# Kernel tuning notes

Measured on AMD Instinct MI355X. Metric: run time of the kernel, lower is better.

## Reference

```python
import jax, jax.numpy as jnp
import numpy as np

B, S, F = 128, 256, 40
H, D, NH, L, FF = 64, 128, 4, 2, 2048
REG, BIN, NW = 8, 1, 3
NEG = -1e9


def _ln(x, s, b, eps=1e-5):
    m = x.mean(-1, keepdims=True)
    v = ((x - m) ** 2).mean(-1, keepdims=True)
    return (x - m) / jnp.sqrt(v + eps) * s + b


def setup_inputs() -> dict:
    key = jax.random.key(0)
    ks = list(jax.random.split(key, 40))
    k = iter(ks)
    def rn(shape, s=0.05):
        return jax.random.normal(next(k), shape, jnp.float32) * s
    inp = {}
    inp['x'] = jax.random.normal(next(k), (B, S, F), jnp.float32)
    inp['mask'] = jnp.ones((B, S, F), jnp.float32)
    inp['delta'] = jax.random.uniform(next(k), (B, S, F), jnp.float32)
    # GRU params (torch layout: [3H, in], gates order r,z,n)
    inp['gru_w_ih'] = rn((3 * H, 3 * F))
    inp['gru_w_hh'] = rn((3 * H, H))
    inp['gru_b_ih'] = rn((3 * H,))
    inp['gru_b_hh'] = rn((3 * H,))
    inp['dm_w'] = rn((D, H)); inp['dm_b'] = rn((D,))
    # transformer layers stacked on leading dim L
    inp['in_proj_w'] = rn((L, 3 * D, D)); inp['in_proj_b'] = rn((L, 3 * D))
    inp['out_proj_w'] = rn((L, D, D)); inp['out_proj_b'] = rn((L, D))
    inp['lin1_w'] = rn((L, FF, D)); inp['lin1_b'] = rn((L, FF))
    inp['lin2_w'] = rn((L, D, FF)); inp['lin2_b'] = rn((L, D))
    inp['ln1_s'] = jnp.ones((L, D), jnp.float32); inp['ln1_b'] = jnp.zeros((L, D), jnp.float32)
    inp['ln2_s'] = jnp.ones((L, D), jnp.float32); inp['ln2_b'] = jnp.zeros((L, D), jnp.float32)
    inp['score_w'] = rn((1, D)); inp['score_b'] = rn((1,))
    inp['reg_w'] = rn((NW, REG, D)); inp['reg_b'] = rn((NW, REG))
    inp['bin_w'] = rn((NW, BIN, D)); inp['bin_b'] = rn((NW, BIN))
    inp['window_id'] = jax.random.randint(next(k), (B,), 0, NW, jnp.int32)
    return inp


def reference(x, mask, delta, gru_w_ih, gru_w_hh, gru_b_ih, gru_b_hh, dm_w, dm_b,
              in_proj_w, in_proj_b, out_proj_w, out_proj_b, lin1_w, lin1_b,
              lin2_w, lin2_b, ln1_s, ln1_b, ln2_s, ln2_b, score_w, score_b,
              reg_w, reg_b, bin_w, bin_b, window_id):
    inp = jnp.concatenate([x, mask, delta], -1)          # [B,S,3F]
    xw = inp @ gru_w_ih.T + gru_b_ih                      # [B,S,3H] precomputed input gates

    def step(h, xw_t):
        gh = h @ gru_w_hh.T + gru_b_hh
        xr, xz, xn = jnp.split(xw_t, 3, -1)
        hr, hz, hn = jnp.split(gh, 3, -1)
        r = jax.nn.sigmoid(xr + hr)
        zg = jax.nn.sigmoid(xz + hz)
        n = jnp.tanh(xn + r * hn)
        h_new = (1.0 - zg) * n + zg * h
        return h_new, h_new

    h0 = jnp.zeros((x.shape[0], H), x.dtype)
    _, hs = jax.lax.scan(step, h0, jnp.swapaxes(xw, 0, 1))  # [S,B,H]
    z = jnp.swapaxes(hs, 0, 1) @ dm_w.T + dm_b              # [B,S,D]

    time_mask = mask.sum(-1) > 0                            # [B,S] bool
    bias = jnp.where(time_mask[:, None, None, :], 0.0, NEG).astype(z.dtype)
    dh = D // NH
    scale = 1.0 / np.sqrt(dh)

    for l in range(L):  # post-LN torch TransformerEncoderLayer
        qkv = z @ in_proj_w[l].T + in_proj_b[l]
        q, k, v = jnp.split(qkv, 3, -1)
        q = q.reshape(B, S, NH, dh).transpose(0, 2, 1, 3)
        k = k.reshape(B, S, NH, dh).transpose(0, 2, 1, 3)
        v = v.reshape(B, S, NH, dh).transpose(0, 2, 1, 3)
        attn = jax.nn.softmax(jnp.einsum('bhqd,bhkd->bhqk', q, k) * scale + bias, -1)
        o = jnp.einsum('bhqk,bhkd->bhqd', attn, v).transpose(0, 2, 1, 3).reshape(B, S, D)
        z = _ln(z + (o @ out_proj_w[l].T + out_proj_b[l]), ln1_s[l], ln1_b[l])
        ff = jax.nn.relu(z @ lin1_w[l].T + lin1_b[l]) @ lin2_w[l].T + lin2_b[l]
        z = _ln(z + ff, ln2_s[l], ln2_b[l])

    scores = (z @ score_w.T + score_b)[..., 0]              # [B,S]
    scores = jnp.where(time_mask, scores, NEG)
    alpha = jax.nn.softmax(scores, 1)
    pooled = jnp.einsum('bsd,bs->bd', z, alpha)             # [B,D]

    # routed heads: gather 1-of-3 head weights per sample, batched matvec
    y_reg = jnp.einsum('bod,bd->bo', reg_w[window_id], pooled) + reg_b[window_id]
    y_bin = jnp.einsum('bod,bd->bo', bin_w[window_id], pooled) + bin_b[window_id]
    return (y_reg, y_bin)
```

## Files before the change

### kernel.cpp

```cpp
#include <hip/hip_runtime.h>

typedef __attribute__((ext_vector_type(8))) short short8;
typedef __attribute__((ext_vector_type(4))) float f32x4;
typedef unsigned short u16;

#define BB   128
#define SS   256
#define FIN  40
#define HH   64
#define DD   128
#define NHH  4
#define LL   2
#define NEGV (-1e9f)

__device__ __forceinline__ u16 f2b(float f) {
    unsigned u = __float_as_uint(f);
    return (u16)((u + 0x7FFFu + ((u >> 16) & 1u)) >> 16);
}
__device__ __forceinline__ float b2f(u16 u) {
    return __uint_as_float(((unsigned)u) << 16);
}

__device__ __forceinline__ void gl_lds16(const void* g, void* s) {
    __builtin_amdgcn_global_load_lds(
        (const __attribute__((address_space(1))) void*)g,
        (__attribute__((address_space(3))) void*)s, 16, 0, 0);
}

__global__ __launch_bounds__(192) void xw_kernel(const float* __restrict__ x,
                                                 const float* __restrict__ mask,
                                                 const float* __restrict__ delta,
                                                 const float* __restrict__ w_ih,
                                                 const float* __restrict__ b_ih,
                                                 float* __restrict__ xwt) {
    __shared__ float inp[16][120];
    __shared__ float wl[192][21];
    int group = blockIdx.x >> 8;
    int t = blockIdx.x & 255;
    int tid = threadIdx.x;

    for (int idx = tid; idx < 16 * 120; idx += 192) {
        int r = idx / 120, k = idx % 120;
        size_t g = (size_t)(group * 16 + r) * 256 + t;
        float v;
        if (k < 40)      v = x[g * FIN + k];
        else if (k < 80) v = mask[g * FIN + (k - 40)];
        else             v = delta[g * FIN + (k - 80)];
        inp[r][k] = v;
    }

    float acc[16];
#pragma unroll
    for (int r = 0; r < 16; ++r) acc[r] = 0.f;

    for (int kt = 0; kt < 6; ++kt) {
        __syncthreads();
        for (int idx = tid; idx < 192 * 20; idx += 192) {
            int r = idx / 20, k = idx % 20;
            wl[r][k] = w_ih[(size_t)r * 120 + kt * 20 + k];
        }
        __syncthreads();
#pragma unroll
        for (int kk = 0; kk < 20; ++kk) {
            float w = wl[tid][kk];
            int kg = kt * 20 + kk;
#pragma unroll
            for (int r = 0; r < 16; ++r) acc[r] += w * inp[r][kg];
        }
    }
    float bias = b_ih[tid];
    float* o = xwt + ((size_t)(group * 256 + t) * 192 + tid) * 16;
#pragma unroll
    for (int r = 0; r < 16; r += 4) {
        float4 v = {acc[r] + bias, acc[r + 1] + bias, acc[r + 2] + bias, acc[r + 3] + bias};
        *(float4*)&o[r] = v;
    }
}

__device__ __forceinline__ float gru_gate(float xr, float xz, float xn,
                                          float ar, float az, float an, float hold) {
    float r  = 1.f / (1.f + __expf(-(xr + ar)));
    float zg = 1.f / (1.f + __expf(-(xz + az)));
    float nx = xn + r * an;
    float n  = 2.f / (1.f + __expf(-2.f * nx)) - 1.f;
    return (1.f - zg) * n + zg * hold;
}

__global__ __launch_bounds__(512, 1) void pre_kernel(const float* __restrict__ w_hh,
                                                     const float* __restrict__ b_hh,
                                                     const float* __restrict__ xwt,
                                                     u16* __restrict__ hsb,
                                                     const float* __restrict__ dm_w,
                                                     const float* __restrict__ ip_w,
                                                     const float* __restrict__ op_w,
                                                     const float* __restrict__ l1_w,
                                                     const float* __restrict__ l2_w,
                                                     u16* __restrict__ o_dm, u16* __restrict__ o_ip,
                                                     u16* __restrict__ o_op, u16* __restrict__ o_l1,
                                                     u16* __restrict__ o_l2,
                                                     const float* __restrict__ mask,
                                                     float* __restrict__ tm) {
    __shared__ __align__(16) u16 hb[2][16 * 64];
    __shared__ __align__(16) u16 hstage[8][16 * 64];
    int blk = blockIdx.x;
    int tid = threadIdx.x;

    if (blk >= 8) {
        if (blk < 298) {
            int cb = blk - 8;
            const float* s; u16* d; int off;
            if      (cb < 2)   { s = dm_w; d = o_dm; off = cb; }
            else if (cb < 26)  { s = ip_w; d = o_ip; off = cb - 2; }
            else if (cb < 34)  { s = op_w; d = o_op; off = cb - 26; }
            else if (cb < 162) { s = l1_w; d = o_l1; off = cb - 34; }
            else               { s = l2_w; d = o_l2; off = cb - 162; }
            int i = (off * 512 + tid) * 8;
            float4 a = *(const float4*)&s[i];
            float4 b = *(const float4*)&s[i + 4];
            short8 o;
            o[0] = (short)f2b(a.x); o[1] = (short)f2b(a.y); o[2] = (short)f2b(a.z); o[3] = (short)f2b(a.w);
            o[4] = (short)f2b(b.x); o[5] = (short)f2b(b.y); o[6] = (short)f2b(b.z); o[7] = (short)f2b(b.w);
            *(short8*)&d[i] = o;
        } else {
            int row = (blk - 298) * 512 + tid;
            if (row < BB * SS) {
                const float* m = mask + (size_t)row * FIN;
                float s = 0.f;
                for (int f = 0; f < FIN; ++f) s += m[f];
                tm[row] = (s > 0.f) ? 1.f : 0.f;
            }
        }
        return;
    }

    int b0 = blk * 16;
    int w = tid >> 6, lane = tid & 63;
    int fr = lane & 15, hi = lane >> 4;
    int cw = w & 3;
    int jg = w >> 2;

    for (int idx = tid; idx < 1024; idx += 512) hb[0][idx] = 0;

    int c = cw * 16 + fr;
    float br_ = b_hh[c], bz_ = b_hh[64 + c], bn_ = b_hh[128 + c];

    short8 wfr[2], wfz[2], wfn[2];
#pragma unroll
    for (int ks = 0; ks < 2; ++ks) {
        int slot = ks * 4 + hi;
        const float* p0 = w_hh + (size_t)c * 64 + slot * 8;
        const float* p1 = w_hh + (size_t)(64 + c) * 64 + slot * 8;
        const float* p2 = w_hh + (size_t)(128 + c) * 64 + slot * 8;
#pragma unroll
        for (int q = 0; q < 8; ++q) {
            wfr[ks][q] = (short)f2b(p0[q]);
            wfz[ks][q] = (short)f2b(p1[q]);
            wfn[ks][q] = (short)f2b(p2[q]);
        }
    }

    const float* xg = xwt + (size_t)blk * (256 * 192 * 16);
    int lo = hi * 4 + jg * 2;

    float hrA = 0.f, hrB = 0.f;

    int woA = (lo + 0) * 64 + ((((c >> 3) ^ ((lo + 0) & 7))) << 3) + (c & 7);
    int woB = (lo + 1) * 64 + ((((c >> 3) ^ ((lo + 1) & 7))) << 3) + (c & 7);
    int soA = (lo + 0) * 64 + c;
    int soB = (lo + 1) * 64 + c;

    float2 pxr[4], pxz[4], pxn[4];
#pragma unroll
    for (int u = 0; u < 4; ++u) {
        pxr[u] = *(const float2*)&xg[((size_t)u * 192 + c) * 16 + lo];
        pxz[u] = *(const float2*)&xg[((size_t)u * 192 + 64 + c) * 16 + lo];
        pxn[u] = *(const float2*)&xg[((size_t)u * 192 + 128 + c) * 16 + lo];
    }
    __syncthreads();

    int cur = 0;
    auto step = [&](float2 xr2, float2 xz2, float2 xn2, int ts) {
        f32x4 ar = {br_, br_, br_, br_};
        f32x4 az = {bz_, bz_, bz_, bz_};
        f32x4 an = {bn_, bn_, bn_, bn_};
#pragma unroll
        for (int ks = 0; ks < 2; ++ks) {
            int soff = (((ks << 2) + hi) ^ (fr & 7)) << 3;
            short8 af = *(const short8*)&hb[cur][fr * 64 + soff];
            ar = __builtin_amdgcn_mfma_f32_16x16x32_bf16(af, wfr[ks], ar, 0, 0, 0);
            az = __builtin_amdgcn_mfma_f32_16x16x32_bf16(af, wfz[ks], az, 0, 0, 0);
            an = __builtin_amdgcn_mfma_f32_16x16x32_bf16(af, wfn[ks], an, 0, 0, 0);
        }
        float aR0, aR1, aZ0, aZ1, aN0, aN1;
        if (jg == 0) { aR0 = ar[0]; aR1 = ar[1]; aZ0 = az[0]; aZ1 = az[1]; aN0 = an[0]; aN1 = an[1]; }
        else         { aR0 = ar[2]; aR1 = ar[3]; aZ0 = az[2]; aZ1 = az[3]; aN0 = an[2]; aN1 = an[3]; }
        hrA = gru_gate(xr2.x, xz2.x, xn2.x, aR0, aZ0, aN0, hrA);
        hrB = gru_gate(xr2.y, xz2.y, xn2.y, aR1, aZ1, aN1, hrB);
        u16 v0 = f2b(hrA), v1 = f2b(hrB);
        int nxt = cur ^ 1;
        hb[nxt][woA] = v0; hb[nxt][woB] = v1;
        hstage[ts][soA] = v0; hstage[ts][soB] = v1;
        asm volatile("s_waitcnt lgkmcnt(0)\n\ts_barrier" ::: "memory");
        cur = nxt;
    };

    for (int t = 0; t < SS; t += 8) {
#pragma unroll
        for (int u = 0; u < 8; ++u) {
            int tp = t + u + 4; tp = (tp < SS) ? tp : (SS - 1);
            float2 nr = *(const float2*)&xg[((size_t)tp * 192 + c) * 16 + lo];
            float2 nz = *(const float2*)&xg[((size_t)tp * 192 + 64 + c) * 16 + lo];
            float2 nn = *(const float2*)&xg[((size_t)tp * 192 + 128 + c) * 16 + lo];
            step(pxr[u & 3], pxz[u & 3], pxn[u & 3], u);
            pxr[u & 3] = nr; pxz[u & 3] = nz; pxn[u & 3] = nn;
        }
#pragma unroll
        for (int f = 0; f < 2; ++f) {
            int idx = tid + f * 512;
            int c8 = idx & 7, pair = idx >> 3;
            int ts = pair >> 4, row = pair & 15;
            short8 v = *(const short8*)&hstage[ts][row * 64 + c8 * 8];
            *(short8*)&hsb[((size_t)(b0 + row) * SS + t + ts) * 64 + c8 * 8] = v;
        }
        asm volatile("s_waitcnt lgkmcnt(0)\n\ts_barrier" ::: "memory");
    }
}

__global__ __launch_bounds__(256, 1) void dmqkv_kernel(const u16* __restrict__ hsb,
                                                       const u16* __restrict__ dmw,
                                                       const float* __restrict__ dmb,
                                                       const u16* __restrict__ ipw,
                                                       const float* __restrict__ ipb,
                                                       float* __restrict__ z,
                                                       u16* __restrict__ qkvb) {
    __shared__ __align__(16) u16 ZB[2][128 * 64];
    __shared__ __align__(16) u16 W1C[2][128 * 64];
    int bm = blockIdx.x;
    int tid = threadIdx.x;
    int w = tid >> 6, lane = tid & 63;
    int wrow = (w >> 1) * 64, wcol = (w & 1) * 64;
    int fr = lane & 15, hi = lane >> 4;
    int rl = lane >> 3, ssl = (lane & 7) ^ rl;
    int swz = fr & 7;

#pragma unroll
    for (int i = 0; i < 4; ++i) {
        int ch = w * 4 + i, row = ch * 8 + rl;
        gl_lds16(hsb + ((size_t)(bm * 128 + row)) * 64 + ssl * 8, &ZB[0][ch * 512]);
        gl_lds16(dmw + ((size_t)row) * 64 + ssl * 8, &W1C[0][ch * 512]);
    }
    __syncthreads();

    f32x4 acc[4][4];
#pragma unroll
    for (int m = 0; m < 4; ++m)
#pragma unroll
        for (int n = 0; n < 4; ++n) acc[m][n] = (f32x4){0.f, 0.f, 0.f, 0.f};
#pragma unroll
    for (int kk = 0; kk < 2; ++kk) {
        int soff = (((kk << 2) + hi) ^ swz) << 3;
        short8 a[4], b[4];
#pragma unroll
        for (int m = 0; m < 4; ++m)
            a[m] = *(const short8*)&ZB[0][(wrow + m * 16 + fr) * 64 + soff];
#pragma unroll
        for (int n = 0; n < 4; ++n)
            b[n] = *(const short8*)&W1C[0][(wcol + n * 16 + fr) * 64 + soff];
#pragma unroll
        for (int m = 0; m < 4; ++m)
#pragma unroll
            for (int n = 0; n < 4; ++n)
                acc[m][n] = __builtin_amdgcn_mfma_f32_16x16x32_bf16(a[m], b[n], acc[m][n], 0, 0, 0);
    }
    __syncthreads();

    float bv[4];
#pragma unroll
    for (int n = 0; n < 4; ++n) bv[n] = dmb[wcol + n * 16 + fr];
#pragma unroll
    for (int m = 0; m < 4; ++m)
#pragma unroll
        for (int j = 0; j < 4; ++j) {
            int lrow = wrow + m * 16 + hi * 4 + j;
            int row = bm * 128 + lrow;
#pragma unroll
            for (int n = 0; n < 4; ++n) {
                int col = wcol + n * 16 + fr;
                float o = acc[m][n][j] + bv[n];
                z[(size_t)row * 128 + col] = o;
                int e = col & 63;
                ZB[col >> 6][lrow * 64 + ((((e >> 3) ^ (lrow & 7))) << 3) + (e & 7)] = f2b(o);
            }
        }
    __syncthreads();

    for (int bn = 0; bn < 3; ++bn) {
#pragma unroll
        for (int hk = 0; hk < 2; ++hk)
#pragma unroll
            for (int i = 0; i < 4; ++i) {
                int ch = w * 4 + i, row = ch * 8 + rl;
                gl_lds16(ipw + ((size_t)(bn * 128 + row)) * 128 + hk * 64 + ssl * 8, &W1C[hk][ch * 512]);
            }
        __syncthreads();

        f32x4 aq[4][4];
#pragma unroll
        for (int m = 0; m < 4; ++m)
#pragma unroll
            for (int n = 0; n < 4; ++n) aq[m][n] = (f32x4){0.f, 0.f, 0.f, 0.f};
#pragma unroll
        for (int ks = 0; ks < 4; ++ks) {
            int hk = ks >> 1;
            int soff = ((((ks & 1) << 2) + hi) ^ swz) << 3;
            short8 a[4], b[4];
#pragma unroll
            for (int m = 0; m < 4; ++m)
                a[m] = *(const short8*)&ZB[hk][(wrow + m * 16 + fr) * 64 + soff];
#pragma unroll
            for (int n = 0; n < 4; ++n)
                b[n] = *(const short8*)&W1C[hk][(wcol + n * 16 + fr) * 64 + soff];
#pragma unroll
            for (int m = 0; m < 4; ++m)
#pragma unroll
                for (int n = 0; n < 4; ++n)
                    aq[m][n] = __builtin_amdgcn_mfma_f32_16x16x32_bf16(a[m], b[n], aq[m][n], 0, 0, 0);
        }
        float qb[4];
#pragma unroll
        for (int n = 0; n < 4; ++n) qb[n] = ipb[bn * 128 + wcol + n * 16 + fr];
#pragma unroll
        for (int m = 0; m < 4; ++m)
#pragma unroll
            for (int j = 0; j < 4; ++j) {
                int row = bm * 128 + wrow + m * 16 + hi * 4 + j;
#pragma unroll
                for (int n = 0; n < 4; ++n)
                    qkvb[(size_t)row * 384 + bn * 128 + wcol + n * 16 + fr] = f2b(aq[m][n][j] + qb[n]);
            }
        __syncthreads();
    }
}

template <bool DO_QKV>
__global__ __launch_bounds__(256, 1) void tailqkv_kernel(const u16* __restrict__ attnob,
                                                         const u16* __restrict__ opw,
                                                         const float* __restrict__ opb,
                                                         const float* __restrict__ ln1s,
                                                         const float* __restrict__ ln1b,
                                                         const u16* __restrict__ w1,
                                                         const float* __restrict__ b1,
                                                         const u16* __restrict__ w2,
                                                         const float* __restrict__ b2,
                                                         const float* __restrict__ lns,
                                                         const float* __restrict__ lnb,
                                                         const u16* __restrict__ ipw,
                                                         const float* __restrict__ ipb,
                                                         float* __restrict__ z,
                                                         u16* __restrict__ qkvb) {
    __shared__ __align__(16) u16 ZB[2][128 * 64];
    __shared__ __align__(16) u16 W1C[2][128 * 64];
    __shared__ __align__(16) u16 W2C[2][128 * 64];
    __shared__ __align__(16) u16 A1[2][128 * 64];
    __shared__ float lred[2][2][128];
    int bm = blockIdx.x;
    int tid = threadIdx.x;
    int w = tid >> 6, lane = tid & 63;
    int wrow = (w >> 1) * 64, wcol = (w & 1) * 64;
    int fr = lane & 15, hi = lane >> 4;
    int rl = lane >> 3, ssl = (lane & 7) ^ rl;
    int swz = fr & 7;
    int xh = wrow >> 6;

#pragma unroll
    for (int hk = 0; hk < 2; ++hk)
#pragma unroll
        for (int i = 0; i < 4; ++i) {
            int ch = w * 4 + i, row = ch * 8 + rl;
            gl_lds16(attnob + ((size_t)(bm * 128 + row)) * 128 + hk * 64 + ssl * 8, &ZB[hk][ch * 512]);
            gl_lds16(opw + ((size_t)row) * 128 + hk * 64 + ssl * 8, &W1C[hk][ch * 512]);
        }
    __syncthreads();

    {
        f32x4 acc1[4][4];
#pragma unroll
        for (int m = 0; m < 4; ++m)
#pragma unroll
            for (int n = 0; n < 4; ++n) acc1[m][n] = (f32x4){0.f, 0.f, 0.f, 0.f};
#pragma unroll
        for (int ks = 0; ks < 4; ++ks) {
            int hk = ks >> 1;
            int soff = ((((ks & 1) << 2) + hi) ^ swz) << 3;
            short8 a[4], b[4];
#pragma unroll
            for (int m = 0; m < 4; ++m)
                a[m] = *(const short8*)&ZB[hk][(wrow + m * 16 + fr) * 64 + soff];
#pragma unroll
            for (int n = 0; n < 4; ++n)
                b[n] = *(const short8*)&W1C[hk][(wcol + n * 16 + fr) * 64 + soff];
#pragma unroll
            for (int m = 0; m < 4; ++m)
#pragma unroll
                for (int n = 0; n < 4; ++n)
                    acc1[m][n] = __builtin_amdgcn_mfma_f32_16x16x32_bf16(a[m], b[n], acc1[m][n], 0, 0, 0);
        }

        float bv[4];
#pragma unroll
        for (int n = 0; n < 4; ++n) bv[n] = opb[wcol + n * 16 + fr];
        float v[4][4][4];
#pragma unroll
        for (int m = 0; m < 4; ++m)
#pragma unroll
            for (int j = 0; j < 4; ++j) {
                int row = bm * 128 + wrow + m * 16 + hi * 4 + j;
#pragma unroll
                for (int n = 0; n < 4; ++n)
                    v[m][n][j] = acc1[m][n][j] + bv[n] + z[(size_t)row * 128 + wcol + n * 16 + fr];
            }
#pragma unroll
        for (int m = 0; m < 4; ++m)
#pragma unroll
            for (int j = 0; j < 4; ++j) {
                float s = v[m][0][j] + v[m][1][j] + v[m][2][j] + v[m][3][j];
                float q = v[m][0][j]*v[m][0][j] + v[m][1][j]*v[m][1][j]
                        + v[m][2][j]*v[m][2][j] + v[m][3][j]*v[m][3][j];
#pragma unroll
                for (int off = 1; off <= 8; off <<= 1) {
                    s += __shfl_xor(s, off);
                    q += __shfl_xor(q, off);
                }
                if (fr == 0) {
                    int lrow = wrow + m * 16 + hi * 4 + j;
                    lred[0][w & 1][lrow] = s;
                    lred[1][w & 1][lrow] = q;
                }
            }
        __syncthreads();
        float sv[4], bb[4];
#pragma unroll
        for (int n = 0; n < 4; ++n) {
            sv[n] = ln1s[wcol + n * 16 + fr];
            bb[n] = ln1b[wcol + n * 16 + fr];
        }
#pragma unroll
        for (int m = 0; m < 4; ++m)
#pragma unroll
            for (int j = 0; j < 4; ++j) {
                int lrow = wrow + m * 16 + hi * 4 + j;
                float mean = (lred[0][0][lrow] + lred[0][1][lrow]) * (1.f / 128.f);
                float msq  = (lred[1][0][lrow] + lred[1][1][lrow]) * (1.f / 128.f);
                float rstd = rsqrtf(msq - mean * mean + 1e-5f);
                int row = bm * 128 + lrow;
#pragma unroll
                for (int n = 0; n < 4; ++n) {
                    int col = wcol + n * 16 + fr;
                    float o = (v[m][n][j] - mean) * rstd * sv[n] + bb[n];
                    z[(size_t)row * 128 + col] = o;
                    int e = col & 63;
                    ZB[col >> 6][lrow * 64 + ((((e >> 3) ^ (lrow & 7))) << 3) + (e & 7)] = f2b(o);
                }
            }
    }
    __syncthreads();

    f32x4 acc2[4][4];
#pragma unroll
    for (int m = 0; m < 4; ++m)
#pragma unroll
        for (int n = 0; n < 4; ++n) acc2[m][n] = (f32x4){0.f, 0.f, 0.f, 0.f};

    for (int ci = 0; ci < 16; ++ci) {
#pragma unroll
        for (int hk = 0; hk < 2; ++hk)
#pragma unroll
            for (int i = 0; i < 4; ++i) {
                int ch = w * 4 + i, row = ch * 8 + rl;
                gl_lds16(w1 + ((size_t)(ci * 128 + row)) * 128 + hk * 64 + ssl * 8, &W1C[hk][ch * 512]);
                gl_lds16(w2 + ((size_t)row) * 2048 + ci * 128 + hk * 64 + ssl * 8, &W2C[hk][ch * 512]);
            }
        __syncthreads();

        f32x4 acc1[4][4];
#pragma unroll
        for (int m = 0; m < 4; ++m)
#pragma unroll
            for (int n = 0; n < 4; ++n) acc1[m][n] = (f32x4){0.f, 0.f, 0.f, 0.f};
#pragma unroll
        for (int ks = 0; ks < 4; ++ks) {
            int hk = ks >> 1;
            int soff = ((((ks & 1) << 2) + hi) ^ swz) << 3;
            short8 a[4], b[4];
#pragma unroll
            for (int m = 0; m < 4; ++m)
                a[m] = *(const short8*)&W1C[hk][(wrow + m * 16 + fr) * 64 + soff];
#pragma unroll
            for (int n = 0; n < 4; ++n)
                b[n] = *(const short8*)&ZB[hk][(wcol + n * 16 + fr) * 64 + soff];
#pragma unroll
            for (int m = 0; m < 4; ++m)
#pragma unroll
                for (int n = 0; n < 4; ++n)
                    acc1[m][n] = __builtin_amdgcn_mfma_f32_16x16x32_bf16(a[m], b[n], acc1[m][n], 0, 0, 0);
        }
#pragma unroll
        for (int m = 0; m < 4; ++m) {
            int x0 = wrow + m * 16 + hi * 4;
            float4 bb = *(const float4*)&b1[ci * 128 + x0];
            int slot = (x0 & 63) >> 3;
            int wadd = x0 & 7;
#pragma unroll
            for (int n = 0; n < 4; ++n) {
                int r = wcol + n * 16 + fr;
                float v0 = fmaxf(acc1[m][n][0] + bb.x, 0.f);
                float v1 = fmaxf(acc1[m][n][1] + bb.y, 0.f);
                float v2 = fmaxf(acc1[m][n][2] + bb.z, 0.f);
                float v3 = fmaxf(acc1[m][n][3] + bb.w, 0.f);
                uint2 pk;
                pk.x = (unsigned)f2b(v0) | ((unsigned)f2b(v1) << 16);
                pk.y = (unsigned)f2b(v2) | ((unsigned)f2b(v3) << 16);
                *(uint2*)&A1[xh][r * 64 + ((slot ^ (r & 7)) << 3) + wadd] = pk;
            }
        }
        __syncthreads();

#pragma unroll
        for (int ks = 0; ks < 4; ++ks) {
            int hk = ks >> 1;
            int soff = ((((ks & 1) << 2) + hi) ^ swz) << 3;
            short8 a[4], b[4];
#pragma unroll
            for (int m = 0; m < 4; ++m)
                a[m] = *(const short8*)&W2C[hk][(wrow + m * 16 + fr) * 64 + soff];
#pragma unroll
            for (int n = 0; n < 4; ++n)
                b[n] = *(const short8*)&A1[hk][(wcol + n * 16 + fr) * 64 + soff];
#pragma unroll
            for (int m = 0; m < 4; ++m)
#pragma unroll
                for (int n = 0; n < 4; ++n)
                    acc2[m][n] = __builtin_amdgcn_mfma_f32_16x16x32_bf16(a[m], b[n], acc2[m][n], 0, 0, 0);
        }
        __syncthreads();
    }

    float vv[4][4][4];
#pragma unroll
    for (int m = 0; m < 4; ++m) {
        int x0 = wrow + m * 16 + hi * 4;
        float4 bb = *(const float4*)&b2[x0];
#pragma unroll
        for (int n = 0; n < 4; ++n) {
            int y = wcol + n * 16 + fr;
            float4 zo = *(const float4*)&z[((size_t)(bm * 128 + y)) * 128 + x0];
            vv[m][n][0] = acc2[m][n][0] + bb.x + zo.x;
            vv[m][n][1] = acc2[m][n][1] + bb.y + zo.y;
            vv[m][n][2] = acc2[m][n][2] + bb.z + zo.z;
            vv[m][n][3] = acc2[m][n][3] + bb.w + zo.w;
        }
    }
#pragma unroll
    for (int n = 0; n < 4; ++n) {
        float s = 0.f, q = 0.f;
#pragma unroll
        for (int m = 0; m < 4; ++m)
#pragma unroll
            for (int j = 0; j < 4; ++j) { float v = vv[m][n][j]; s += v; q += v * v; }
        s += __shfl_xor(s, 16); s += __shfl_xor(s, 32);
        q += __shfl_xor(q, 16); q += __shfl_xor(q, 32);
        if (hi == 0) {
            int y = wcol + n * 16 + fr;
            lred[0][xh][y] = s;
            lred[1][xh][y] = q;
        }
    }
    __syncthreads();
#pragma unroll
    for (int n = 0; n < 4; ++n) {
        int y = wcol + n * 16 + fr;
        float mean = (lred[0][0][y] + lred[0][1][y]) * (1.f / 128.f);
        float msq  = (lred[1][0][y] + lred[1][1][y]) * (1.f / 128.f);
        float rstd = rsqrtf(msq - mean * mean + 1e-5f);
#pragma unroll
        for (int m = 0; m < 4; ++m) {
            int x0 = wrow + m * 16 + hi * 4;
            float4 sv = *(const float4*)&lns[x0];
            float4 bv = *(const float4*)&lnb[x0];
            float o0 = (vv[m][n][0] - mean) * rstd * sv.x + bv.x;
            float o1 = (vv[m][n][1] - mean) * rstd * sv.y + bv.y;
            float o2 = (vv[m][n][2] - mean) * rstd * sv.z + bv.z;
            float o3 = (vv[m][n][3] - mean) * rstd * sv.w + bv.w;
            size_t zoff = ((size_t)(bm * 128 + y)) * 128 + x0;
            *(float4*)&z[zoff] = (float4){o0, o1, o2, o3};
            if (DO_QKV) {
#pragma unroll
                for (int j = 0; j < 4; ++j) {
                    int col = x0 + j;
                    int e = col & 63;
                    float ov = (j == 0) ? o0 : (j == 1) ? o1 : (j == 2) ? o2 : o3;
                    ZB[col >> 6][y * 64 + ((((e >> 3) ^ (y & 7))) << 3) + (e & 7)] = f2b(ov);
                }
            }
        }
    }

    if (DO_QKV) {
        __syncthreads();
        for (int bn = 0; bn < 3; ++bn) {
#pragma unroll
            for (int hk = 0; hk < 2; ++hk)
#pragma unroll
                for (int i = 0; i < 4; ++i) {
                    int ch = w * 4 + i, row = ch * 8 + rl;
                    gl_lds16(ipw + ((size_t)(bn * 128 + row)) * 128 + hk * 64 + ssl * 8, &W1C[hk][ch * 512]);
                }
            __syncthreads();

            f32x4 aq[4][4];
#pragma unroll
            for (int m = 0; m < 4; ++m)
#pragma unroll
                for (int n = 0; n < 4; ++n) aq[m][n] = (f32x4){0.f, 0.f, 0.f, 0.f};
#pragma unroll
            for (int ks = 0; ks < 4; ++ks) {
                int hk = ks >> 1;
                int soff = ((((ks & 1) << 2) + hi) ^ swz) << 3;
                short8 a[4], b[4];
#pragma unroll
                for (int m = 0; m < 4; ++m)
                    a[m] = *(const short8*)&ZB[hk][(wrow + m * 16 + fr) * 64 + soff];
#pragma unroll
                for (int n = 0; n < 4; ++n)
                    b[n] = *(const short8*)&W1C[hk][(wcol + n * 16 + fr) * 64 + soff];
#pragma unroll
                for (int m = 0; m < 4; ++m)
#pragma unroll
                    for (int n = 0; n < 4; ++n)
                        aq[m][n] = __builtin_amdgcn_mfma_f32_16x16x32_bf16(a[m], b[n], aq[m][n], 0, 0, 0);
            }
            float qb[4];
#pragma unroll
            for (int n = 0; n < 4; ++n) qb[n] = ipb[bn * 128 + wcol + n * 16 + fr];
#pragma unroll
            for (int m = 0; m < 4; ++m)
#pragma unroll
                for (int j = 0; j < 4; ++j) {
                    int row = bm * 128 + wrow + m * 16 + hi * 4 + j;
#pragma unroll
                    for (int n = 0; n < 4; ++n)
                        qkvb[(size_t)row * 384 + bn * 128 + wcol + n * 16 + fr] = f2b(aq[m][n][j] + qb[n]);
                }
            __syncthreads();
        }
    }
}

__global__ __launch_bounds__(256) void attn_mfma_kernel(const u16* __restrict__ qkv,
                                                        const float* __restrict__ tm,
                                                        u16* __restrict__ attno) {
    __shared__ __align__(16) u16 Kl[256 * 40];
    __shared__ __align__(16) u16 Vt[32 * 264];
    __shared__ __align__(16) u16 Pl[4][64 * 72];
    __shared__ float tmb[256];
    int bh = blockIdx.x;
    int b = bh >> 2, hd = bh & 3;
    int tid = threadIdx.x;
    int w = tid >> 6, lane = tid & 63;
    int fr = lane & 15, hi = lane >> 4;
    const u16* base = qkv + (size_t)b * SS * 384 + hd * 32;

    for (int idx = tid; idx < 1024; idx += 256) {
        int r = idx >> 2, s = idx & 3;
        short8 v = *(const short8*)(base + (size_t)r * 384 + 128 + s * 8);
        *(short8*)&Kl[r * 40 + s * 8] = v;
    }
    for (int idx = tid; idx < 1024; idx += 256) {
        int r = idx >> 2, s = idx & 3;
        short8 v = *(const short8*)(base + (size_t)r * 384 + 256 + s * 8);
#pragma unroll
        for (int q = 0; q < 8; ++q) Vt[(s * 8 + q) * 264 + r] = (u16)v[q];
    }
    tmb[tid] = (tm[b * SS + tid] > 0.f) ? 0.f : NEGV;

    int q0 = w * 64;
    short8 qf[4];
#pragma unroll
    for (int m = 0; m < 4; ++m)
        qf[m] = *(const short8*)(base + (size_t)(q0 + m * 16 + fr) * 384 + hi * 8);
    __syncthreads();

    const float scale = 0.17677669529663687f;
    f32x4 accO[4][2];
#pragma unroll
    for (int m = 0; m < 4; ++m) {
        accO[m][0] = (f32x4){0.f, 0.f, 0.f, 0.f};
        accO[m][1] = (f32x4){0.f, 0.f, 0.f, 0.f};
    }
    float den[4][4];
#pragma unroll
    for (int m = 0; m < 4; ++m)
#pragma unroll
        for (int j = 0; j < 4; ++j) den[m][j] = 0.f;

    u16* pw = &Pl[w][0];

    for (int kt = 0; kt < 4; ++kt) {
        f32x4 accS[4][4];
#pragma unroll
        for (int m = 0; m < 4; ++m)
#pragma unroll
            for (int n = 0; n < 4; ++n) accS[m][n] = (f32x4){0.f, 0.f, 0.f, 0.f};
        short8 kf[4];
#pragma unroll
        for (int n = 0; n < 4; ++n)
            kf[n] = *(const short8*)&Kl[(kt * 64 + n * 16 + fr) * 40 + hi * 8];
#pragma unroll
        for (int m = 0; m < 4; ++m)
#pragma unroll
            for (int n = 0; n < 4; ++n)
                accS[m][n] = __builtin_amdgcn_mfma_f32_16x16x32_bf16(qf[m], kf[n], accS[m][n], 0, 0, 0);

        float bias[4];
#pragma unroll
        for (int n = 0; n < 4; ++n) bias[n] = tmb[kt * 64 + n * 16 + fr];

#pragma unroll
        for (int m = 0; m < 4; ++m) {
            float rs0 = 0.f, rs1 = 0.f, rs2 = 0.f, rs3 = 0.f;
#pragma unroll
            for (int n = 0; n < 4; ++n) {
                float p0 = __expf(accS[m][n][0] * scale + bias[n]);
                float p1 = __expf(accS[m][n][1] * scale + bias[n]);
                float p2 = __expf(accS[m][n][2] * scale + bias[n]);
                float p3 = __expf(accS[m][n][3] * scale + bias[n]);
                rs0 += p0; rs1 += p1; rs2 += p2; rs3 += p3;
                int cb = n * 16 + fr;
                pw[(m * 16 + hi * 4 + 0) * 72 + cb] = f2b(p0);
                pw[(m * 16 + hi * 4 + 1) * 72 + cb] = f2b(p1);
                pw[(m * 16 + hi * 4 + 2) * 72 + cb] = f2b(p2);
                pw[(m * 16 + hi * 4 + 3) * 72 + cb] = f2b(p3);
            }
#pragma unroll
            for (int off = 1; off <= 8; off <<= 1) {
                rs0 += __shfl_xor(rs0, off);
                rs1 += __shfl_xor(rs1, off);
                rs2 += __shfl_xor(rs2, off);
                rs3 += __shfl_xor(rs3, off);
            }
            den[m][0] += rs0; den[m][1] += rs1; den[m][2] += rs2; den[m][3] += rs3;
        }
        asm volatile("s_waitcnt lgkmcnt(0)" ::: "memory");

#pragma unroll
        for (int ks = 0; ks < 2; ++ks) {
            short8 pf[4], vf[2];
#pragma unroll
            for (int m = 0; m < 4; ++m)
                pf[m] = *(const short8*)&pw[(m * 16 + fr) * 72 + ks * 32 + hi * 8];
#pragma unroll
            for (int nd = 0; nd < 2; ++nd)
                vf[nd] = *(const short8*)&Vt[(nd * 16 + fr) * 264 + kt * 64 + ks * 32 + hi * 8];
#pragma unroll
            for (int m = 0; m < 4; ++m)
#pragma unroll
                for (int nd = 0; nd < 2; ++nd)
                    accO[m][nd] = __builtin_amdgcn_mfma_f32_16x16x32_bf16(pf[m], vf[nd], accO[m][nd], 0, 0, 0);
        }
    }

    u16* orow = attno + (size_t)(b * SS + q0) * DD + hd * 32;
#pragma unroll
    for (int m = 0; m < 4; ++m)
#pragma unroll
        for (int j = 0; j < 4; ++j) {
            float inv = 1.f / den[m][j];
            int qr = m * 16 + hi * 4 + j;
            orow[(size_t)qr * DD + fr]      = f2b(accO[m][0][j] * inv);
            orow[(size_t)qr * DD + 16 + fr] = f2b(accO[m][1][j] * inv);
        }
}

__global__ __launch_bounds__(256) void pool_all_kernel(const float* __restrict__ z,
                                                       const float* __restrict__ score_w,
                                                       const float* __restrict__ score_b,
                                                       const float* __restrict__ tm,
                                                       const float* __restrict__ reg_w,
                                                       const float* __restrict__ reg_b,
                                                       const float* __restrict__ bin_w,
                                                       const float* __restrict__ bin_b,
                                                       const int* __restrict__ wid,
                                                       float* __restrict__ out) {
    int b = blockIdx.x;
    int tid = threadIdx.x;
    __shared__ float sw[128];
    __shared__ float al[SS];
    __shared__ float red[8];
    __shared__ float pp[2][128];
    __shared__ float p[128];

    if (tid < 128) sw[tid] = score_w[tid];
    __syncthreads();

    const float* zr = z + ((size_t)b * SS + tid) * DD;
    float acc = 0.f;
#pragma unroll
    for (int j = 0; j < 128; j += 4) {
        float4 a = *(const float4*)&zr[j];
        float4 wv = *(const float4*)&sw[j];
        acc += a.x * wv.x + a.y * wv.y + a.z * wv.z + a.w * wv.w;
    }
    float sc = acc + score_b[0];
    sc = (tm[b * SS + tid] > 0.f) ? sc : NEGV;

    float m = sc;
#pragma unroll
    for (int off = 32; off; off >>= 1) m = fmaxf(m, __shfl_xor(m, off));
    if ((tid & 63) == 0) red[tid >> 6] = m;
    __syncthreads();
    m = fmaxf(fmaxf(red[0], red[1]), fmaxf(red[2], red[3]));
    float e = __expf(sc - m);
    float ssum = e;
#pragma unroll
    for (int off = 32; off; off >>= 1) ssum += __shfl_xor(ssum, off);
    if ((tid & 63) == 0) red[4 + (tid >> 6)] = ssum;
    __syncthreads();
    ssum = red[4] + red[5] + red[6] + red[7];
    al[tid] = e / ssum;
    __syncthreads();

    int d = tid & 127, half = tid >> 7;
    float pa = 0.f;
    for (int t = half; t < SS; t += 2) pa += al[t] * z[((size_t)b * SS + t) * DD + d];
    pp[half][d] = pa;
    __syncthreads();
    if (tid < 128) p[tid] = pp[0][tid] + pp[1][tid];
    __syncthreads();

    if (tid < 9) {
        int wi = wid[b];
        const float* wrow;
        float bias;
        if (tid < 8) { wrow = reg_w + ((size_t)wi * 8 + tid) * 128; bias = reg_b[wi * 8 + tid]; }
        else         { wrow = bin_w + (size_t)wi * 128;             bias = bin_b[wi]; }
        float hacc = bias;
        for (int k = 0; k < 128; ++k) hacc += wrow[k] * p[k];
        if (tid < 8) out[b * 8 + tid] = hacc;
        else         out[1024 + b] = hacc;
    }
}

extern "C" void kernel_launch(void* const* d_in, const int* in_sizes, int n_in,
                              void* d_out, int out_size, void* d_ws, size_t ws_size,
                              hipStream_t stream) {
    const float* x         = (const float*)d_in[0];
    const float* mask      = (const float*)d_in[1];
    const float* delta     = (const float*)d_in[2];
    const float* gru_w_ih  = (const float*)d_in[3];
    const float* gru_w_hh  = (const float*)d_in[4];
    const float* gru_b_ih  = (const float*)d_in[5];
    const float* gru_b_hh  = (const float*)d_in[6];
    const float* dm_w      = (const float*)d_in[7];
    const float* dm_b      = (const float*)d_in[8];
    const float* in_proj_w = (const float*)d_in[9];
    const float* in_proj_b = (const float*)d_in[10];
    const float* out_proj_w= (const float*)d_in[11];
    const float* out_proj_b= (const float*)d_in[12];
    const float* lin1_w    = (const float*)d_in[13];
    const float* lin1_b    = (const float*)d_in[14];
    const float* lin2_w    = (const float*)d_in[15];
    const float* lin2_b    = (const float*)d_in[16];
    const float* ln1_s     = (const float*)d_in[17];
    const float* ln1_bb    = (const float*)d_in[18];
    const float* ln2_s     = (const float*)d_in[19];
    const float* ln2_bb    = (const float*)d_in[20];
    const float* score_w   = (const float*)d_in[21];
    const float* score_b   = (const float*)d_in[22];
    const float* reg_w     = (const float*)d_in[23];
    const float* reg_b     = (const float*)d_in[24];
    const float* bin_w     = (const float*)d_in[25];
    const float* bin_b     = (const float*)d_in[26];
    const int*   window_id = (const int*)d_in[27];
    float* out = (float*)d_out;

    char* w8 = (char*)d_ws;
    float* z      = (float*)(w8 + 0);
    u16*   hsb    = (u16*)  (w8 + 25165824);
    u16*   wb_dm  = (u16*)  (w8 + 29360128);
    u16*   wb_ip  = (u16*)  (w8 + 29376512);
    u16*   wb_op  = (u16*)  (w8 + 29573120);
    u16*   wb_l1  = (u16*)  (w8 + 29638656);
    u16*   wb_l2  = (u16*)  (w8 + 30687232);
    float* tm     = (float*)(w8 + 31735808);
    float* xwt    = (float*)(w8 + 32063488);
    u16*   qkvb   = (u16*)  (w8 + 32063488);
    u16*   attnob = (u16*)  (w8 + 57229312);

    xw_kernel<<<2048, 192, 0, stream>>>(x, mask, delta, gru_w_ih, gru_b_ih, xwt);
    pre_kernel<<<362, 512, 0, stream>>>(gru_w_hh, gru_b_hh, xwt, hsb,
                                        dm_w, in_proj_w, out_proj_w, lin1_w, lin2_w,
                                        wb_dm, wb_ip, wb_op, wb_l1, wb_l2, mask, tm);

    dmqkv_kernel<<<256, 256, 0, stream>>>(hsb, wb_dm, dm_b, wb_ip, in_proj_b, z, qkvb);

    attn_mfma_kernel<<<BB * NHH, 256, 0, stream>>>(qkvb, tm, attnob);
    tailqkv_kernel<true><<<256, 256, 0, stream>>>(
        attnob, wb_op, out_proj_b, ln1_s, ln1_bb,
        wb_l1, lin1_b, wb_l2, lin2_b, ln2_s, ln2_bb,
        wb_ip + 49152, in_proj_b + 384, z, qkvb);

    attn_mfma_kernel<<<BB * NHH, 256, 0, stream>>>(qkvb, tm, attnob);
    tailqkv_kernel<false><<<256, 256, 0, stream>>>(
        attnob, wb_op + 16384, out_proj_b + 128, ln1_s + 128, ln1_bb + 128,
        wb_l1 + 262144, lin1_b + 2048, wb_l2 + 262144, lin2_b + 128,
        ln2_s + 128, ln2_bb + 128, nullptr, nullptr, z, nullptr);

    pool_all_kernel<<<BB, 256, 0, stream>>>(z, score_w, score_b, tm,
                                            reg_w, reg_b, bin_w, bin_b, window_id, out);
}
```

Before: 484.2 us.

## Run GRU recurrence per-wavefront with register hidden state and no barriers

The GRU recurrence is restructured so each wavefront independently handles two batch rows across all 64 hidden units. The hidden state lives in registers and is redistributed with ds_bpermute, instead of being exchanged through LDS with a block-wide barrier every timestep. The xw precompute output layout changes to match the per-wave, two-row slicing. This spreads the serial recurrence over 64 waves instead of 8 blocks and removes per-step barriers. In exchange each step does more MFMAs, because most of each 16-row tile is wasted on 2 real rows, plus extra shuffles, uses more registers, and writes hsb with narrow 16-bit stores.

```diff
diff --git a/kernel.cpp b/kernel.cpp
--- a/kernel.cpp
+++ b/kernel.cpp
@@ -69,11 +69,10 @@
         }
     }
     float bias = b_ih[tid];
-    float* o = xwt + ((size_t)(group * 256 + t) * 192 + tid) * 16;
-#pragma unroll
-    for (int r = 0; r < 16; r += 4) {
-        float4 v = {acc[r] + bias, acc[r + 1] + bias, acc[r + 2] + bias, acc[r + 3] + bias};
-        *(float4*)&o[r] = v;
+#pragma unroll
+    for (int p = 0; p < 8; ++p) {
+        float2 v = {acc[2 * p] + bias, acc[2 * p + 1] + bias};
+        *(float2*)&xwt[(((size_t)(group * 8 + p) * 256 + t) * 192 + tid) * 2] = v;
     }
 }
 
@@ -86,7 +85,7 @@
     return (1.f - zg) * n + zg * hold;
 }
 
-__global__ __launch_bounds__(512, 1) void pre_kernel(const float* __restrict__ w_hh,
+__global__ __launch_bounds__(256, 1) void pre_kernel(const float* __restrict__ w_hh,
                                                      const float* __restrict__ b_hh,
                                                      const float* __restrict__ xwt,
                                                      u16* __restrict__ hsb,
@@ -100,21 +99,19 @@
                                                      u16* __restrict__ o_l2,
                                                      const float* __restrict__ mask,
                                                      float* __restrict__ tm) {
-    __shared__ __align__(16) u16 hb[2][16 * 64];
-    __shared__ __align__(16) u16 hstage[8][16 * 64];
     int blk = blockIdx.x;
     int tid = threadIdx.x;
 
-    if (blk >= 8) {
-        if (blk < 298) {
-            int cb = blk - 8;
+    if (blk >= 16) {
+        if (blk < 596) {
+            int cb = blk - 16;
             const float* s; u16* d; int off;
-            if      (cb < 2)   { s = dm_w; d = o_dm; off = cb; }
-            else if (cb < 26)  { s = ip_w; d = o_ip; off = cb - 2; }
-            else if (cb < 34)  { s = op_w; d = o_op; off = cb - 26; }
-            else if (cb < 162) { s = l1_w; d = o_l1; off = cb - 34; }
-            else               { s = l2_w; d = o_l2; off = cb - 162; }
-            int i = (off * 512 + tid) * 8;
+            if      (cb < 4)   { s = dm_w; d = o_dm; off = cb; }
+            else if (cb < 52)  { s = ip_w; d = o_ip; off = cb - 4; }
+            else if (cb < 68)  { s = op_w; d = o_op; off = cb - 52; }
+            else if (cb < 324) { s = l1_w; d = o_l1; off = cb - 68; }
+            else               { s = l2_w; d = o_l2; off = cb - 324; }
+            int i = (off * 256 + tid) * 8;
             float4 a = *(const float4*)&s[i];
             float4 b = *(const float4*)&s[i + 4];
             short8 o;
@@ -122,7 +119,7 @@
             o[4] = (short)f2b(b.x); o[5] = (short)f2b(b.y); o[6] = (short)f2b(b.z); o[7] = (short)f2b(b.w);
             *(short8*)&d[i] = o;
         } else {
-            int row = (blk - 298) * 512 + tid;
+            int row = (blk - 596) * 256 + tid;
             if (row < BB * SS) {
                 const float* m = mask + (size_t)row * FIN;
                 float s = 0.f;
@@ -133,96 +130,94 @@
         return;
     }
 
-    int b0 = blk * 16;
     int w = tid >> 6, lane = tid & 63;
-    int fr = lane & 15, hi = lane >> 4;
-    int cw = w & 3;
-    int jg = w >> 2;
-
-    for (int idx = tid; idx < 1024; idx += 512) hb[0][idx] = 0;
-
-    int c = cw * 16 + fr;
-    float br_ = b_hh[c], bz_ = b_hh[64 + c], bn_ = b_hh[128 + c];
-
-    short8 wfr[2], wfz[2], wfn[2];
-#pragma unroll
-    for (int ks = 0; ks < 2; ++ks) {
-        int slot = ks * 4 + hi;
-        const float* p0 = w_hh + (size_t)c * 64 + slot * 8;
-        const float* p1 = w_hh + (size_t)(64 + c) * 64 + slot * 8;
-        const float* p2 = w_hh + (size_t)(128 + c) * 64 + slot * 8;
-#pragma unroll
-        for (int q = 0; q < 8; ++q) {
-            wfr[ks][q] = (short)f2b(p0[q]);
-            wfz[ks][q] = (short)f2b(p1[q]);
-            wfn[ks][q] = (short)f2b(p2[q]);
-        }
-    }
-
-    const float* xg = xwt + (size_t)blk * (256 * 192 * 16);
-    int lo = hi * 4 + jg * 2;
-
-    float hrA = 0.f, hrB = 0.f;
-
-    int woA = (lo + 0) * 64 + ((((c >> 3) ^ ((lo + 0) & 7))) << 3) + (c & 7);
-    int woB = (lo + 1) * 64 + ((((c >> 3) ^ ((lo + 1) & 7))) << 3) + (c & 7);
-    int soA = (lo + 0) * 64 + c;
-    int soB = (lo + 1) * 64 + c;
-
-    float2 pxr[4], pxz[4], pxn[4];
-#pragma unroll
-    for (int u = 0; u < 4; ++u) {
-        pxr[u] = *(const float2*)&xg[((size_t)u * 192 + c) * 16 + lo];
-        pxz[u] = *(const float2*)&xg[((size_t)u * 192 + 64 + c) * 16 + lo];
-        pxn[u] = *(const float2*)&xg[((size_t)u * 192 + 128 + c) * 16 + lo];
-    }
-    __syncthreads();
-
-    int cur = 0;
-    auto step = [&](float2 xr2, float2 xz2, float2 xn2, int ts) {
-        f32x4 ar = {br_, br_, br_, br_};
-        f32x4 az = {bz_, bz_, bz_, bz_};
-        f32x4 an = {bn_, bn_, bn_, bn_};
-#pragma unroll
-        for (int ks = 0; ks < 2; ++ks) {
-            int soff = (((ks << 2) + hi) ^ (fr & 7)) << 3;
-            short8 af = *(const short8*)&hb[cur][fr * 64 + soff];
-            ar = __builtin_amdgcn_mfma_f32_16x16x32_bf16(af, wfr[ks], ar, 0, 0, 0);
-            az = __builtin_amdgcn_mfma_f32_16x16x32_bf16(af, wfz[ks], az, 0, 0, 0);
-            an = __builtin_amdgcn_mfma_f32_16x16x32_bf16(af, wfn[ks], an, 0, 0, 0);
-        }
-        float aR0, aR1, aZ0, aZ1, aN0, aN1;
-        if (jg == 0) { aR0 = ar[0]; aR1 = ar[1]; aZ0 = az[0]; aZ1 = az[1]; aN0 = an[0]; aN1 = an[1]; }
-        else         { aR0 = ar[2]; aR1 = ar[3]; aZ0 = az[2]; aZ1 = az[3]; aN0 = an[2]; aN1 = an[3]; }
-        hrA = gru_gate(xr2.x, xz2.x, xn2.x, aR0, aZ0, aN0, hrA);
-        hrB = gru_gate(xr2.y, xz2.y, xn2.y, aR1, aZ1, aN1, hrB);
-        u16 v0 = f2b(hrA), v1 = f2b(hrB);
-        int nxt = cur ^ 1;
-        hb[nxt][woA] = v0; hb[nxt][woB] = v1;
-        hstage[ts][soA] = v0; hstage[ts][soB] = v1;
-        asm volatile("s_waitcnt lgkmcnt(0)\n\ts_barrier" ::: "memory");
-        cur = nxt;
-    };
+    int hi = lane >> 4, fr = lane & 15;
+    int P = blk * 4 + w;
+    int b0 = P * 2;
+
+    float bgn[3][4];
+#pragma unroll
+    for (int g = 0; g < 3; ++g)
+#pragma unroll
+        for (int n = 0; n < 4; ++n) bgn[g][n] = b_hh[g * 64 + n * 16 + fr];
+
+    short8 wf[3][4][2];
+#pragma unroll
+    for (int g = 0; g < 3; ++g)
+#pragma unroll
+        for (int n = 0; n < 4; ++n)
+#pragma unroll
+            for (int ks = 0; ks < 2; ++ks) {
+                const float* p = w_hh + (size_t)(g * 64 + n * 16 + fr) * 64 + ks * 32 + hi * 8;
+#pragma unroll
+                for (int q = 0; q < 8; ++q) wf[g][n][ks][q] = (short)f2b(p[q]);
+            }
+
+    const float* xg = xwt + (size_t)P * (256 * 192 * 2);
+
+    float2 px[4][3];
+#pragma unroll
+    for (int u = 0; u < 4; ++u)
+#pragma unroll
+        for (int g = 0; g < 3; ++g)
+            px[u][g] = *(const float2*)&xg[((size_t)u * 192 + g * 64 + lane) * 2];
+
+    unsigned hp = 0;
+    float h0 = 0.f, h1 = 0.f;
+    unsigned hs[8];
 
     for (int t = 0; t < SS; t += 8) {
 #pragma unroll
         for (int u = 0; u < 8; ++u) {
             int tp = t + u + 4; tp = (tp < SS) ? tp : (SS - 1);
-            float2 nr = *(const float2*)&xg[((size_t)tp * 192 + c) * 16 + lo];
-            float2 nz = *(const float2*)&xg[((size_t)tp * 192 + 64 + c) * 16 + lo];
-            float2 nn = *(const float2*)&xg[((size_t)tp * 192 + 128 + c) * 16 + lo];
-            step(pxr[u & 3], pxz[u & 3], pxn[u & 3], u);
-            pxr[u & 3] = nr; pxz[u & 3] = nz; pxn[u & 3] = nn;
-        }
-#pragma unroll
-        for (int f = 0; f < 2; ++f) {
-            int idx = tid + f * 512;
-            int c8 = idx & 7, pair = idx >> 3;
-            int ts = pair >> 4, row = pair & 15;
-            short8 v = *(const short8*)&hstage[ts][row * 64 + c8 * 8];
-            *(short8*)&hsb[((size_t)(b0 + row) * SS + t + ts) * 64 + c8 * 8] = v;
-        }
-        asm volatile("s_waitcnt lgkmcnt(0)\n\ts_barrier" ::: "memory");
+            float2 n0 = *(const float2*)&xg[((size_t)tp * 192 + lane) * 2];
+            float2 n1 = *(const float2*)&xg[((size_t)tp * 192 + 64 + lane) * 2];
+            float2 n2 = *(const float2*)&xg[((size_t)tp * 192 + 128 + lane) * 2];
+
+            short8 af0, af1;
+#pragma unroll
+            for (int q = 0; q < 8; ++q) {
+                int v0 = __builtin_amdgcn_ds_bpermute((hi * 8 + q) << 2, (int)hp);
+                int v1 = __builtin_amdgcn_ds_bpermute((32 + hi * 8 + q) << 2, (int)hp);
+                af0[q] = (short)((fr & 1) ? ((unsigned)v0 >> 16) : ((unsigned)v0 & 0xffffu));
+                af1[q] = (short)((fr & 1) ? ((unsigned)v1 >> 16) : ((unsigned)v1 & 0xffffu));
+            }
+
+            f32x4 acc[3][4];
+#pragma unroll
+            for (int g = 0; g < 3; ++g)
+#pragma unroll
+                for (int n = 0; n < 4; ++n) {
+                    acc[g][n] = (f32x4){bgn[g][n], bgn[g][n], bgn[g][n], bgn[g][n]};
+                    acc[g][n] = __builtin_amdgcn_mfma_f32_16x16x32_bf16(af0, wf[g][n][0], acc[g][n], 0, 0, 0);
+                    acc[g][n] = __builtin_amdgcn_mfma_f32_16x16x32_bf16(af1, wf[g][n][1], acc[g][n], 0, 0, 0);
+                }
+
+            float gh[3][2];
+#pragma unroll
+            for (int g = 0; g < 3; ++g)
+#pragma unroll
+                for (int r = 0; r < 2; ++r) {
+                    float t0 = __shfl(acc[g][0][r], fr);
+                    float t1 = __shfl(acc[g][1][r], fr);
+                    float t2 = __shfl(acc[g][2][r], fr);
+                    float t3 = __shfl(acc[g][3][r], fr);
+                    gh[g][r] = (hi == 0) ? t0 : (hi == 1) ? t1 : (hi == 2) ? t2 : t3;
+                }
+
+            float2 xr2 = px[u & 3][0], xz2 = px[u & 3][1], xn2 = px[u & 3][2];
+            h0 = gru_gate(xr2.x, xz2.x, xn2.x, gh[0][0], gh[1][0], gh[2][0], h0);
+            h1 = gru_gate(xr2.y, xz2.y, xn2.y, gh[0][1], gh[1][1], gh[2][1], h1);
+            hp = (unsigned)f2b(h0) | ((unsigned)f2b(h1) << 16);
+            hs[u] = hp;
+
+            px[u & 3][0] = n0; px[u & 3][1] = n1; px[u & 3][2] = n2;
+        }
+#pragma unroll
+        for (int ts = 0; ts < 8; ++ts) {
+            hsb[((size_t)b0 * SS + t + ts) * 64 + lane]       = (u16)(hs[ts] & 0xffffu);
+            hsb[((size_t)(b0 + 1) * SS + t + ts) * 64 + lane] = (u16)(hs[ts] >> 16);
+        }
     }
 }
 
@@ -897,7 +892,7 @@
     u16*   attnob = (u16*)  (w8 + 57229312);
 
     xw_kernel<<<2048, 192, 0, stream>>>(x, mask, delta, gru_w_ih, gru_b_ih, xwt);
-    pre_kernel<<<362, 512, 0, stream>>>(gru_w_hh, gru_b_hh, xwt, hsb,
+    pre_kernel<<<724, 256, 0, stream>>>(gru_w_hh, gru_b_hh, xwt, hsb,
                                         dm_w, in_proj_w, out_proj_w, lin1_w, lin2_w,
                                         wb_dm, wb_ip, wb_op, wb_l1, wb_l2, mask, tm);
 
```

Result: slower. 534.7 us (+10.4%).
